# Kernel optimization log

Hardware: AMD Instinct MI355X
Metric: run time of the kernel (lower is better)

The kernel has to match this reference:

```python
import jax, jax.numpy as jnp
import numpy as np
from jax import lax

T = 16384          # num_tokens
H = 512            # hidden_size
HC = 4             # hc_mult
NGRAM = 4          # max_ngram_size -> conv dilation
N_EMBED = 256      # n_embed_per_ngram
N_HEADPN = 4       # n_head_per_ngram
NUM_HEADS = (NGRAM - 1) * N_HEADPN          # 12 embedding heads
HEAD_DIM = N_EMBED // N_HEADPN              # 64
E = (NGRAM - 1) * N_EMBED                   # 768 = engram_hidden_size
VOCAB = 50000
K = 4              # conv kernel_size
EPS = 1e-5         # layernorm_eps
GATE_EPS = 1e-6


def setup_inputs() -> dict:
    key = jax.random.key(0)
    ks = jax.random.split(key, 8)
    hash_ids = jax.random.randint(ks[0], (T, NUM_HEADS), 0, VOCAB, dtype=jnp.int32)
    offsets = jnp.asarray(np.concatenate([[0], np.cumsum([VOCAB] * (NUM_HEADS - 1))]).astype(np.int32))
    embedding_weight = jax.random.normal(ks[1], (NUM_HEADS * VOCAB, HEAD_DIM), jnp.float32) * 0.02
    key_projs_w = jax.random.normal(ks[2], (HC, E, H), jnp.float32) * 0.02
    q_norm_w = jnp.ones((HC, H), jnp.float32)
    k_norm_w = jnp.ones((HC, H), jnp.float32)
    v_proj_w = jax.random.normal(ks[3], (E, H), jnp.float32) * 0.02
    conv_w = jax.random.normal(ks[4], (HC * H, K), jnp.float32) * 0.1
    conv_norm_w = jnp.ones((HC, H), jnp.float32)
    hidden_states = jax.random.normal(ks[5], (T, HC, H), jnp.float32)
    return {
        'hash_ids': hash_ids, 'offsets': offsets, 'embedding_weight': embedding_weight,
        'key_projs_w': key_projs_w, 'q_norm_w': q_norm_w, 'k_norm_w': k_norm_w,
        'v_proj_w': v_proj_w, 'conv_w': conv_w, 'conv_norm_w': conv_norm_w,
        'hidden_states': hidden_states,
    }


def _group_rms_norm(x, w, eps=EPS):
    # x: [G, T, H], w: [G, H]; RMS over last dim, per-group affine scale
    inv = lax.rsqrt(jnp.mean(x * x, axis=-1, keepdims=True) + eps)
    return x * inv * w[:, None, :]


def reference(hash_ids, offsets, embedding_weight, key_projs_w, q_norm_w, k_norm_w,
              v_proj_w, conv_w, conv_norm_w, hidden_states):
    num_tokens, hc_mult, hidden = hidden_states.shape
    # --- MultiHeadEmbedding: hash-indexed gather into a concatenated table ---
    emb = embedding_weight[hash_ids + offsets[None, :]]          # [T, NUM_HEADS, HEAD_DIM]
    emb = emb.reshape(num_tokens, E)                              # [T, E]
    # --- key projection per hc group (bmm) ---
    keys = jnp.einsum('te,geh->gth', emb, key_projs_w)            # [HC, T, H]
    key_n = _group_rms_norm(keys, k_norm_w)
    query_n = _group_rms_norm(hidden_states.transpose(1, 0, 2), q_norm_w)  # [HC, T, H]
    # --- scaled dot-product gate ---
    scale = 1.0 / jnp.sqrt(jnp.asarray(hidden, hidden_states.dtype))
    gate = jax.nn.sigmoid(jnp.sum(key_n * query_n, axis=-1) * scale)       # [HC, T]
    gate = gate.T[:, :, None]                                     # [T, HC, 1]
    # --- value projection + gating ---
    value = gate * (emb @ v_proj_w)[:, None, :]                   # [T, HC, H]
    # --- ShortConv: GroupRMSNorm + depthwise dilated causal conv1d + SiLU ---
    x_n = _group_rms_norm(value.transpose(1, 0, 2), conv_norm_w)  # [HC, T, H]
    x_bct = x_n.transpose(0, 2, 1).reshape(1, hc_mult * hidden, num_tokens)  # [1, C, T]
    pad = NGRAM * (K - 1)
    y = lax.conv_general_dilated(
        x_bct, conv_w[:, None, :],                                # kernel [C, 1, K]
        window_strides=(1,), padding=[(pad, 0)], rhs_dilation=(NGRAM,),
        feature_group_count=hc_mult * hidden,
        dimension_numbers=('NCH', 'OIH', 'NCH'))
    y = jax.nn.silu(y)[0]                                         # [C, T]
    y = y.reshape(hc_mult, hidden, num_tokens).transpose(2, 0, 1) # [T, HC, H]
    return value + y


if __name__ == '__main__':
    out = reference(**setup_inputs())
    print(out.shape, out.dtype)
```

## Files before the change

### kernel.cpp

```cpp
#include <hip/hip_runtime.h>
#include <hip/hip_bf16.h>
#include <math.h>

#define T_TOK  16384
#define H_DIM  512
#define NHEADS 12
#define E_DIM  768
#define EPS_N  1e-5f
#define QK_SCALE 0.04419417382415922f

typedef unsigned short u16;
typedef __bf16 bf16;
typedef bf16   bf16x8 __attribute__((ext_vector_type(8)));
typedef float  f32x4  __attribute__((ext_vector_type(4)));
typedef u16    u16x4  __attribute__((ext_vector_type(4)));
typedef u16    u16x8  __attribute__((ext_vector_type(8)));

__device__ __forceinline__ u16 f2bf(float f) {
  unsigned u = __builtin_bit_cast(unsigned, f);
  unsigned r = u + 0x7fffu + ((u >> 16) & 1u);
  return (u16)(r >> 16);
}
__device__ __forceinline__ float bf2f(u16 h) {
  unsigned u = ((unsigned)h) << 16;
  return __builtin_bit_cast(float, u);
}
__device__ __forceinline__ float wave_sum(float v) {
  #pragma unroll
  for (int off = 32; off; off >>= 1) v += __shfl_xor(v, off, 64);
  return v;
}

__global__ __launch_bounds__(256) void gather_emb(
    const int* __restrict__ hash_ids, const int* __restrict__ offsets,
    const float* __restrict__ emb_w, u16* __restrict__ emb) {
  int idx = blockIdx.x * 256 + threadIdx.x;
  int pair = idx >> 3;
  int sub = idx & 7;
  int t = pair / 12;
  int head = pair - t * 12;
  int row = hash_ids[pair] + offsets[head];
  const float* src = emb_w + (size_t)row * 64 + sub * 8;
  float4 a = *(const float4*)src;
  float4 b = *(const float4*)(src + 4);
  u16x8 o;
  o[0] = f2bf(a.x); o[1] = f2bf(a.y); o[2] = f2bf(a.z); o[3] = f2bf(a.w);
  o[4] = f2bf(b.x); o[5] = f2bf(b.y); o[6] = f2bf(b.z); o[7] = f2bf(b.w);
  *(u16x8*)(emb + (size_t)t * E_DIM + head * 64 + sub * 8) = o;
}

__global__ __launch_bounds__(256) void build_wcat(
    const float* __restrict__ kp, const float* __restrict__ vp,
    u16* __restrict__ wt) {
  __shared__ float tile[32][33];
  int m = blockIdx.z;
  const float* src = (m < 4) ? (kp + (size_t)m * E_DIM * H_DIM) : vp;
  int h0 = blockIdx.x * 32, e0 = blockIdx.y * 32;
  int tx = threadIdx.x, ty = threadIdx.y;
  #pragma unroll
  for (int j = 0; j < 32; j += 8)
    tile[ty + j][tx] = src[(size_t)(e0 + ty + j) * H_DIM + h0 + tx];
  __syncthreads();
  #pragma unroll
  for (int j = 0; j < 32; j += 8) {
    int h = h0 + ty + j, e = e0 + tx;
    wt[(size_t)(m * H_DIM + h) * E_DIM + e] = f2bf(tile[tx][ty + j]);
  }
}

__global__ __launch_bounds__(256) void build_wc(
    const float* __restrict__ conv_w, const float* __restrict__ cnw,
    const float* __restrict__ qw, const float* __restrict__ kw,
    float* __restrict__ wc, float* __restrict__ qwkw) {
  int cf = blockIdx.x * 256 + threadIdx.x;
  float c = cnw[cf];
  #pragma unroll
  for (int k = 0; k < 4; ++k) wc[k * 2048 + cf] = conv_w[cf * 4 + k] * c;
  qwkw[cf] = qw[cf] * kw[cf];
}

__global__ __launch_bounds__(256) void prep_q(
    const float* __restrict__ hidden, const float* __restrict__ qwkw,
    u16* __restrict__ qhp, float* __restrict__ qssA) {
  __shared__ u16 qs[32 * 72];
  int t = blockIdx.x, tid = threadIdx.x;
  int b = tid >> 3;
  int c0 = tid * 8;
  const float* hp = hidden + (size_t)t * 2048 + c0;
  float4 a0 = *(const float4*)hp;
  float4 a1 = *(const float4*)(hp + 4);
  float4 w0 = *(const float4*)(qwkw + c0);
  float4 w1 = *(const float4*)(qwkw + c0 + 4);
  float q[8] = {a0.x, a0.y, a0.z, a0.w, a1.x, a1.y, a1.z, a1.w};
  float w[8] = {w0.x, w0.y, w0.z, w0.w, w1.x, w1.y, w1.z, w1.w};
  float q2 = 0.f;
  u16x8 v;
  #pragma unroll
  for (int j = 0; j < 8; ++j) { q2 += q[j] * q[j]; v[j] = f2bf(q[j] * w[j]); }
  *(u16x8*)&qs[b * 72 + (c0 & 63)] = v;
  q2 = wave_sum(q2);
  if ((tid & 63) == 0) qssA[t * 4 + (tid >> 6)] = q2;
  __syncthreads();
  int r0 = (c0 & 63) >> 2;
  u16x8 o;
  #pragma unroll
  for (int half = 0; half < 2; ++half)
    #pragma unroll
    for (int j = 0; j < 4; ++j)
      o[half * 4 + j] = qs[b * 72 + j * 16 + r0 + half];
  *(u16x8*)(qhp + (size_t)t * 2048 + c0) = o;
}

__global__ __launch_bounds__(256, 2) void gemm_bf16(
    const u16* __restrict__ A, const u16* __restrict__ BT,
    const u16* __restrict__ qhp,
    u16* __restrict__ V, float* __restrict__ kssP, float* __restrict__ qkP,
    float* __restrict__ msvP) {
  __shared__ char smem[32768];
  u16 (*As)[64] = (u16(*)[64])smem;
  u16 (*Bs)[64] = (u16(*)[64])(smem + 16384);
  float2* red2 = (float2*)smem;
  float*  red1 = (float*)smem;
  const int K = E_DIM;
  int tid = threadIdx.x;
  int lane = tid & 63, wid = tid >> 6;
  int bx = blockIdx.x, by = blockIdx.y;
  int wm = (wid >> 1) * 64, wn = (wid & 1) * 64;
  int widN = wid & 1;
  int lr16 = lane & 15, rgrp = lane >> 4;

  const u16* aptr = A + (size_t)(by * 128 + (tid >> 3)) * K + (tid & 7) * 8;
  const u16* bptr = BT + (size_t)(bx * 128 + (tid >> 3)) * K + (tid & 7) * 8;
  int lds_off = tid * 16;

  f32x4 acc[4][4] = {};

  for (int k0 = 0; k0 < K; k0 += 64) {
    #pragma unroll
    for (int r = 0; r < 4; ++r) {
      __builtin_amdgcn_global_load_lds(
        (const __attribute__((address_space(1))) void*)(aptr + (size_t)(r * 32) * K + k0),
        (__attribute__((address_space(3))) void*)(smem + r * 4096 + lds_off),
        16, 0, 0);
      __builtin_amdgcn_global_load_lds(
        (const __attribute__((address_space(1))) void*)(bptr + (size_t)(r * 32) * K + k0),
        (__attribute__((address_space(3))) void*)(smem + 16384 + r * 4096 + lds_off),
        16, 0, 0);
    }
    __syncthreads();
    int lk8 = (lane >> 4) * 8;
    #pragma unroll
    for (int kk = 0; kk < 2; ++kk) {
      bf16x8 af[4], bfv[4];
      #pragma unroll
      for (int m = 0; m < 4; ++m)
        af[m] = *reinterpret_cast<const bf16x8*>(&As[wm + m * 16 + lr16][kk * 32 + lk8]);
      #pragma unroll
      for (int n = 0; n < 4; ++n)
        bfv[n] = *reinterpret_cast<const bf16x8*>(&Bs[wn + n * 16 + lr16][kk * 32 + lk8]);
      #pragma unroll
      for (int m = 0; m < 4; ++m)
        #pragma unroll
        for (int n = 0; n < 4; ++n)
          acc[m][n] = __builtin_amdgcn_mfma_f32_16x16x32_bf16(af[m], bfv[n], acc[m][n], 0, 0, 0);
    }
    __syncthreads();
  }

  if (bx < 16) {
    int g = bx >> 2, qq = bx & 3;
    int cb = (g * 8 + qq * 2 + (wn >> 6)) * 64 + lr16 * 4;
    u16x4 qf[4][4];
    #pragma unroll
    for (int m = 0; m < 4; ++m)
      #pragma unroll
      for (int j = 0; j < 4; ++j)
        qf[m][j] = *(const u16x4*)(qhp +
            (size_t)(by * 128 + wm + m * 16 + rgrp * 4 + j) * 2048 + cb);
    #pragma unroll
    for (int m = 0; m < 4; ++m) {
      #pragma unroll
      for (int j = 0; j < 4; ++j) {
        int r = wm + m * 16 + rgrp * 4 + j;
        float sk2 = 0.f, sqk = 0.f;
        #pragma unroll
        for (int n = 0; n < 4; ++n) {
          float kv = acc[m][n][j];
          sk2 += kv * kv;
          sqk += bf2f(qf[m][j][n]) * kv;
        }
        red2[(widN * 128 + r) * 16 + lr16] = make_float2(sk2, sqk);
      }
    }
    __syncthreads();
    if (tid < 128) {
      float s0 = 0.f, s1 = 0.f;
      #pragma unroll
      for (int j = 0; j < 16; ++j) {
        int jj = (j + tid) & 15;
        float2 a = red2[tid * 16 + jj];
        float2 b = red2[(128 + tid) * 16 + jj];
        s0 += a.x + b.x;
        s1 += a.y + b.y;
      }
      int t = by * 128 + tid;
      int o = (t * 4 + g) * 4 + qq;
      kssP[o] = s0;
      qkP[o]  = s1;
    }
  } else {
    int q2i = bx - 16;
    #pragma unroll
    for (int m = 0; m < 4; ++m) {
      #pragma unroll
      for (int j = 0; j < 4; ++j) {
        int r = wm + m * 16 + rgrp * 4 + j;
        size_t t = (size_t)(by * 128 + r);
        float sv2 = 0.f;
        #pragma unroll
        for (int n = 0; n < 4; ++n) {
          float v = acc[m][n][j];
          sv2 += v * v;
          V[t * 512 + q2i * 128 + wn + n * 16 + lr16] = f2bf(v);
        }
        red1[(widN * 128 + r) * 16 + lr16] = sv2;
      }
    }
    __syncthreads();
    if (tid < 128) {
      float s = 0.f;
      #pragma unroll
      for (int j = 0; j < 16; ++j) {
        int jj = (j + tid) & 15;
        s += red1[tid * 16 + jj] + red1[(128 + tid) * 16 + jj];
      }
      int t = by * 128 + tid;
      msvP[t * 4 + q2i] = s;
    }
  }
}

__global__ __launch_bounds__(256) void gate_finish(
    const float* __restrict__ kssP, const float* __restrict__ qkP,
    const float* __restrict__ qssA, const float* __restrict__ msvP,
    float* __restrict__ gateA, float* __restrict__ aA) {
  int i = blockIdx.x * 256 + threadIdx.x;
  int t = i >> 2;
  float4 k4 = *(const float4*)&kssP[i * 4];
  float4 d4 = *(const float4*)&qkP[i * 4];
  float4 m4 = *(const float4*)&msvP[t * 4];
  float kss = k4.x + k4.y + k4.z + k4.w;
  float qk  = d4.x + d4.y + d4.z + d4.w;
  float qss = qssA[i];
  float msv = (m4.x + m4.y + m4.z + m4.w) * (1.0f / 512.0f);
  float qinv = rsqrtf(qss * (1.0f / 512.0f) + EPS_N);
  float kinv = rsqrtf(kss * (1.0f / 512.0f) + EPS_N);
  float gate = 1.0f / (1.0f + __expf(-qk * qinv * kinv * QK_SCALE));
  gateA[i] = gate;
  aA[i] = gate * rsqrtf(gate * gate * msv + EPS_N);
}

__global__ __launch_bounds__(256) void out_kernel(
    const u16* __restrict__ V,
    const float* __restrict__ gateA, const float* __restrict__ aA,
    const float* __restrict__ wc,
    float* __restrict__ out) {
  int idx = blockIdx.x * 256 + threadIdx.x;
  int t = idx >> 8;
  int c8 = (idx & 255) * 8;
  int g = c8 >> 9;
  int h = c8 & 511;

  float acc[8] = {0.f, 0.f, 0.f, 0.f, 0.f, 0.f, 0.f, 0.f};
  float vr_t[8];
  #pragma unroll
  for (int k = 0; k < 4; ++k) {
    int tk = t - 12 + 4 * k;
    if (tk < 0) continue;
    float s = aA[tk * 4 + g];
    u16x8 vv = *(const u16x8*)&V[(size_t)tk * 512 + h];
    float4 w0 = *(const float4*)(wc + k * 2048 + c8);
    float4 w1 = *(const float4*)(wc + k * 2048 + c8 + 4);
    float w8[8] = {w0.x, w0.y, w0.z, w0.w, w1.x, w1.y, w1.z, w1.w};
    #pragma unroll
    for (int j = 0; j < 8; ++j) {
      float v = bf2f(vv[j]);
      acc[j] += w8[j] * s * v;
      if (k == 3) vr_t[j] = v;
    }
  }
  float gate = gateA[t * 4 + g];
  float r[8];
  #pragma unroll
  for (int j = 0; j < 8; ++j) {
    float y = acc[j];
    r[j] = gate * vr_t[j] + y / (1.0f + __expf(-y));
  }
  float* op = out + (size_t)t * 2048 + c8;
  *(float4*)op       = make_float4(r[0], r[1], r[2], r[3]);
  *(float4*)(op + 4) = make_float4(r[4], r[5], r[6], r[7]);
}

extern "C" void kernel_launch(void* const* d_in, const int* in_sizes, int n_in,
                              void* d_out, int out_size, void* d_ws, size_t ws_size,
                              hipStream_t stream) {
  const int*   hash_ids = (const int*)d_in[0];
  const int*   offsets  = (const int*)d_in[1];
  const float* emb_w    = (const float*)d_in[2];
  const float* kp       = (const float*)d_in[3];
  const float* qw       = (const float*)d_in[4];
  const float* kw       = (const float*)d_in[5];
  const float* vp       = (const float*)d_in[6];
  const float* conv_w   = (const float*)d_in[7];
  const float* cw       = (const float*)d_in[8];
  const float* hidden   = (const float*)d_in[9];
  float* out = (float*)d_out;
  char*  ws  = (char*)d_ws;

  u16*   V     = (u16*)ws;
  u16*   emb   = (u16*)(ws + 16777216);
  u16*   wt    = (u16*)(ws + 41943040);
  u16*   qhp   = (u16*)(ws + 45875200);
  float* kssP  = (float*)(ws + 112984064);
  float* qkP   = (float*)(ws + 114032640);
  float* qssA  = (float*)(ws + 115081216);
  float* msvP  = (float*)(ws + 115343360);
  float* gateA = (float*)(ws + 115605504);
  float* aA    = (float*)(ws + 115867648);
  float* wc    = (float*)(ws + 116129792);
  float* qwkw  = (float*)(ws + 116162560);

  gather_emb<<<(T_TOK * 12 * 8) / 256, 256, 0, stream>>>(hash_ids, offsets, emb_w, emb);
  build_wcat<<<dim3(16, 24, 5), dim3(32, 8), 0, stream>>>(kp, vp, wt);
  build_wc<<<8, 256, 0, stream>>>(conv_w, cw, qw, kw, wc, qwkw);
  prep_q<<<T_TOK, 256, 0, stream>>>(hidden, qwkw, qhp, qssA);
  gemm_bf16<<<dim3(20, 128), 256, 0, stream>>>(emb, wt, qhp, V, kssP, qkP, msvP);
  gate_finish<<<(T_TOK * 4) / 256, 256, 0, stream>>>(kssP, qkP, qssA, msvP, gateA, aA);
  out_kernel<<<T_TOK * 256 / 256, 256, 0, stream>>>(V, gateA, aA, wc, out);
}
```

Baseline: 196.3 us.

## Fuse query prep into GEMM epilogue and swizzle block order

Removes the separate prep_q kernel and its bf16 query staging buffer. The GEMM epilogue now reads hidden states directly, computes partial query sums of squares per 128-column tile, stages the query tile in LDS, and applies qw*kw scaling in registers. It also adds a block-index swizzle so consecutive blocks share B tiles or rows, and halves the LDS reduction with a shuffle. In exchange the kernel uses more LDS (50 KB), which may reduce occupancy, and the epilogue does extra global loads of fp32 hidden data.

```diff
diff --git a/kernel.cpp b/kernel.cpp
--- a/kernel.cpp
+++ b/kernel.cpp
@@ -24,11 +24,6 @@
 __device__ __forceinline__ float bf2f(u16 h) {
   unsigned u = ((unsigned)h) << 16;
   return __builtin_bit_cast(float, u);
-}
-__device__ __forceinline__ float wave_sum(float v) {
-  #pragma unroll
-  for (int off = 32; off; off >>= 1) v += __shfl_xor(v, off, 64);
-  return v;
 }
 
 __global__ __launch_bounds__(256) void gather_emb(
@@ -79,52 +74,25 @@
   qwkw[cf] = qw[cf] * kw[cf];
 }
 
-__global__ __launch_bounds__(256) void prep_q(
-    const float* __restrict__ hidden, const float* __restrict__ qwkw,
-    u16* __restrict__ qhp, float* __restrict__ qssA) {
-  __shared__ u16 qs[32 * 72];
-  int t = blockIdx.x, tid = threadIdx.x;
-  int b = tid >> 3;
-  int c0 = tid * 8;
-  const float* hp = hidden + (size_t)t * 2048 + c0;
-  float4 a0 = *(const float4*)hp;
-  float4 a1 = *(const float4*)(hp + 4);
-  float4 w0 = *(const float4*)(qwkw + c0);
-  float4 w1 = *(const float4*)(qwkw + c0 + 4);
-  float q[8] = {a0.x, a0.y, a0.z, a0.w, a1.x, a1.y, a1.z, a1.w};
-  float w[8] = {w0.x, w0.y, w0.z, w0.w, w1.x, w1.y, w1.z, w1.w};
-  float q2 = 0.f;
-  u16x8 v;
-  #pragma unroll
-  for (int j = 0; j < 8; ++j) { q2 += q[j] * q[j]; v[j] = f2bf(q[j] * w[j]); }
-  *(u16x8*)&qs[b * 72 + (c0 & 63)] = v;
-  q2 = wave_sum(q2);
-  if ((tid & 63) == 0) qssA[t * 4 + (tid >> 6)] = q2;
-  __syncthreads();
-  int r0 = (c0 & 63) >> 2;
-  u16x8 o;
-  #pragma unroll
-  for (int half = 0; half < 2; ++half)
-    #pragma unroll
-    for (int j = 0; j < 4; ++j)
-      o[half * 4 + j] = qs[b * 72 + j * 16 + r0 + half];
-  *(u16x8*)(qhp + (size_t)t * 2048 + c0) = o;
-}
-
 __global__ __launch_bounds__(256, 2) void gemm_bf16(
     const u16* __restrict__ A, const u16* __restrict__ BT,
-    const u16* __restrict__ qhp,
+    const float* __restrict__ hidden, const float* __restrict__ qwkw,
     u16* __restrict__ V, float* __restrict__ kssP, float* __restrict__ qkP,
-    float* __restrict__ msvP) {
-  __shared__ char smem[32768];
+    float* __restrict__ qssP, float* __restrict__ msvP) {
+  __shared__ __align__(16) char smem[50176];
   u16 (*As)[64] = (u16(*)[64])smem;
   u16 (*Bs)[64] = (u16(*)[64])(smem + 16384);
-  float2* red2 = (float2*)smem;
-  float*  red1 = (float*)smem;
+  u16*    qlds  = (u16*)smem;
+  float2* red2h = (float2*)(smem + 33792);
+  float*  red1  = (float*)smem;
   const int K = E_DIM;
   int tid = threadIdx.x;
   int lane = tid & 63, wid = tid >> 6;
-  int bx = blockIdx.x, by = blockIdx.y;
+
+  int orig = blockIdx.x + blockIdx.y * 20;
+  int swz = (orig & 7) * 320 + (orig >> 3);
+  int bx = swz % 20, by = swz / 20;
+
   int wm = (wid >> 1) * 64, wn = (wid & 1) * 64;
   int widN = wid & 1;
   int lr16 = lane & 15, rgrp = lane >> 4;
@@ -169,14 +137,40 @@
 
   if (bx < 16) {
     int g = bx >> 2, qq = bx & 3;
-    int cb = (g * 8 + qq * 2 + (wn >> 6)) * 64 + lr16 * 4;
-    u16x4 qf[4][4];
-    #pragma unroll
-    for (int m = 0; m < 4; ++m)
-      #pragma unroll
-      for (int j = 0; j < 4; ++j)
-        qf[m][j] = *(const u16x4*)(qhp +
-            (size_t)(by * 128 + wm + m * 16 + rgrp * 4 + j) * 2048 + cb);
+    const float* hq = hidden + (size_t)(by * 128) * 2048 + g * 512 + qq * 128;
+    float s2[8];
+    #pragma unroll
+    for (int p = 0; p < 8; ++p) {
+      int row = p * 16 + (tid >> 4);
+      int col = (tid & 15) * 8;
+      const float* src = hq + (size_t)row * 2048 + col;
+      float4 x0 = *(const float4*)src;
+      float4 x1 = *(const float4*)(src + 4);
+      float qv[8] = {x0.x, x0.y, x0.z, x0.w, x1.x, x1.y, x1.z, x1.w};
+      u16x8 o;
+      float ss = 0.f;
+      #pragma unroll
+      for (int j = 0; j < 8; ++j) { ss += qv[j] * qv[j]; o[j] = f2bf(qv[j]); }
+      s2[p] = ss;
+      *(u16x8*)&qlds[row * 132 + col] = o;
+    }
+    #pragma unroll
+    for (int off = 1; off < 16; off <<= 1)
+      #pragma unroll
+      for (int p = 0; p < 8; ++p) s2[p] += __shfl_xor(s2[p], off, 64);
+    if ((tid & 15) == 0) {
+      #pragma unroll
+      for (int p = 0; p < 8; ++p) {
+        int t = by * 128 + p * 16 + (tid >> 4);
+        qssP[(t * 4 + g) * 4 + qq] = s2[p];
+      }
+    }
+    __syncthreads();
+
+    int colg = g * 512 + qq * 128 + wn + lr16;
+    float w4[4];
+    #pragma unroll
+    for (int n = 0; n < 4; ++n) w4[n] = qwkw[colg + n * 16];
     #pragma unroll
     for (int m = 0; m < 4; ++m) {
       #pragma unroll
@@ -186,20 +180,23 @@
         #pragma unroll
         for (int n = 0; n < 4; ++n) {
           float kv = acc[m][n][j];
+          float qv = bf2f(qlds[r * 132 + wn + n * 16 + lr16]);
           sk2 += kv * kv;
-          sqk += bf2f(qf[m][j][n]) * kv;
+          sqk += qv * w4[n] * kv;
         }
-        red2[(widN * 128 + r) * 16 + lr16] = make_float2(sk2, sqk);
+        sk2 += __shfl_xor(sk2, 8, 64);
+        sqk += __shfl_xor(sqk, 8, 64);
+        if (lr16 < 8) red2h[(widN * 128 + r) * 8 + lr16] = make_float2(sk2, sqk);
       }
     }
     __syncthreads();
     if (tid < 128) {
       float s0 = 0.f, s1 = 0.f;
       #pragma unroll
-      for (int j = 0; j < 16; ++j) {
-        int jj = (j + tid) & 15;
-        float2 a = red2[tid * 16 + jj];
-        float2 b = red2[(128 + tid) * 16 + jj];
+      for (int j = 0; j < 8; ++j) {
+        int jj = (j + tid) & 7;
+        float2 a = red2h[tid * 8 + jj];
+        float2 b = red2h[(128 + tid) * 8 + jj];
         s0 += a.x + b.x;
         s1 += a.y + b.y;
       }
@@ -242,16 +239,17 @@
 
 __global__ __launch_bounds__(256) void gate_finish(
     const float* __restrict__ kssP, const float* __restrict__ qkP,
-    const float* __restrict__ qssA, const float* __restrict__ msvP,
+    const float* __restrict__ qssP, const float* __restrict__ msvP,
     float* __restrict__ gateA, float* __restrict__ aA) {
   int i = blockIdx.x * 256 + threadIdx.x;
   int t = i >> 2;
   float4 k4 = *(const float4*)&kssP[i * 4];
   float4 d4 = *(const float4*)&qkP[i * 4];
+  float4 q4 = *(const float4*)&qssP[i * 4];
   float4 m4 = *(const float4*)&msvP[t * 4];
   float kss = k4.x + k4.y + k4.z + k4.w;
   float qk  = d4.x + d4.y + d4.z + d4.w;
-  float qss = qssA[i];
+  float qss = q4.x + q4.y + q4.z + q4.w;
   float msv = (m4.x + m4.y + m4.z + m4.w) * (1.0f / 512.0f);
   float qinv = rsqrtf(qss * (1.0f / 512.0f) + EPS_N);
   float kinv = rsqrtf(kss * (1.0f / 512.0f) + EPS_N);
@@ -320,21 +318,20 @@
   u16*   V     = (u16*)ws;
   u16*   emb   = (u16*)(ws + 16777216);
   u16*   wt    = (u16*)(ws + 41943040);
-  u16*   qhp   = (u16*)(ws + 45875200);
-  float* kssP  = (float*)(ws + 112984064);
-  float* qkP   = (float*)(ws + 114032640);
-  float* qssA  = (float*)(ws + 115081216);
-  float* msvP  = (float*)(ws + 115343360);
-  float* gateA = (float*)(ws + 115605504);
-  float* aA    = (float*)(ws + 115867648);
-  float* wc    = (float*)(ws + 116129792);
-  float* qwkw  = (float*)(ws + 116162560);
+  float* kssP  = (float*)(ws + 45875200);
+  float* qkP   = (float*)(ws + 46923776);
+  float* qssP  = (float*)(ws + 47972352);
+  float* msvP  = (float*)(ws + 49020928);
+  float* gateA = (float*)(ws + 49283072);
+  float* aA    = (float*)(ws + 49545216);
+  float* wc    = (float*)(ws + 49807360);
+  float* qwkw  = (float*)(ws + 49840128);
 
   gather_emb<<<(T_TOK * 12 * 8) / 256, 256, 0, stream>>>(hash_ids, offsets, emb_w, emb);
   build_wcat<<<dim3(16, 24, 5), dim3(32, 8), 0, stream>>>(kp, vp, wt);
   build_wc<<<8, 256, 0, stream>>>(conv_w, cw, qw, kw, wc, qwkw);
-  prep_q<<<T_TOK, 256, 0, stream>>>(hidden, qwkw, qhp, qssA);
-  gemm_bf16<<<dim3(20, 128), 256, 0, stream>>>(emb, wt, qhp, V, kssP, qkP, msvP);
-  gate_finish<<<(T_TOK * 4) / 256, 256, 0, stream>>>(kssP, qkP, qssA, msvP, gateA, aA);
+  gemm_bf16<<<dim3(20, 128), 256, 0, stream>>>(emb, wt, hidden, qwkw,
+                                               V, kssP, qkP, qssP, msvP);
+  gate_finish<<<(T_TOK * 4) / 256, 256, 0, stream>>>(kssP, qkP, qssP, msvP, gateA, aA);
   out_kernel<<<T_TOK * 256 / 256, 256, 0, stream>>>(V, gateA, aA, wc, out);
 }
```

New measurement: 184.0 us. -6.3%, faster.
